# Kernel tuning notes

Measured on AMD Instinct MI355X. Metric: run time of the kernel, lower is better.

## Reference

```python
import jax, jax.numpy as jnp
import numpy as np

WINDOW_SIZE = 11
CHANNEL = 3
SIGMA = 1.5
C1 = 0.01 ** 2
C2 = 0.03 ** 2


def _gaussian_window():
    # 1D gaussian, normalized, then outer product -> [C,1,K,K] depthwise kernel
    x = np.arange(WINDOW_SIZE, dtype=np.float32)
    g = np.exp(-(x - WINDOW_SIZE // 2) ** 2 / (2.0 * SIGMA ** 2))
    g = g / g.sum()
    w2d = np.outer(g, g).astype(np.float32)  # [K,K]
    w = np.broadcast_to(w2d, (CHANNEL, 1, WINDOW_SIZE, WINDOW_SIZE)).copy()
    return jnp.asarray(w)


def _depthwise_conv(x, w):
    # x: [N,C,H,W], w: [C,1,K,K]; SAME padding (pad = K//2, K odd) matches torch
    pad = WINDOW_SIZE // 2
    return jax.lax.conv_general_dilated(
        x, w,
        window_strides=(1, 1),
        padding=((pad, pad), (pad, pad)),
        dimension_numbers=("NCHW", "OIHW", "NCHW"),
        feature_group_count=CHANNEL,
    )


def setup_inputs() -> dict:
    key = jax.random.key(0)
    kA, kB = jax.random.split(key)
    shape = (16, 3, 512, 512)
    A = jax.random.uniform(kA, shape, dtype=jnp.float32)
    B = jax.random.uniform(kB, shape, dtype=jnp.float32)
    return {"A": A, "B": B}


def reference(A, B):
    w = _gaussian_window()
    mu1 = _depthwise_conv(A, w)
    mu2 = _depthwise_conv(B, w)
    mu1_sq = mu1 * mu1
    mu2_sq = mu2 * mu2
    mu12 = mu1 * mu2
    sigma1_sq = _depthwise_conv(A * A, w) - mu1_sq
    sigma2_sq = _depthwise_conv(B * B, w) - mu2_sq
    sigma12 = _depthwise_conv(A * B, w) - mu12
    num = (2.0 * mu12 + C1) * (2.0 * sigma12 + C2)
    den = (mu1_sq + mu2_sq + C1) * (sigma1_sq + sigma2_sq + C2)
    ssim_map = num / den
    return jnp.nanmean(ssim_map)
```

## Files before the change

### kernel.cpp

```cpp
#include <hip/hip_runtime.h>
#include <math.h>


#define TX 64
#define TY 32
#define SR 42
#define HSTRIDE 65
#define IMG_H 512
#define IMG_W 512
#define C1F 1.0e-4f
#define C2F 9.0e-4f

__global__ void ssim_zero(double* acc) { *acc = 0.0; }

__global__ void ssim_finalize(const double* acc, float* out) {
    *out = (float)(*acc / 12582912.0);
}

__global__ __launch_bounds__(256, 3)
void ssim_main(const float* __restrict__ A, const float* __restrict__ B,
               double* __restrict__ acc)
{
    __shared__ float h[5][SR * HSTRIDE];

    const int t  = threadIdx.x;
    const int x0 = blockIdx.x * TX;
    const int y0 = blockIdx.y * TY;
    const size_t pbase = (size_t)blockIdx.z * (size_t)(IMG_H * IMG_W);
    const float* __restrict__ pa = A + pbase;
    const float* __restrict__ pb = B + pbase;

    float g[11];
    {
        float gs = 0.f;
        #pragma unroll
        for (int i = 0; i < 11; ++i) {
            const float d = (float)(i - 5);
            g[i] = expf(-d * d / 4.5f);
            gs += g[i];
        }
        #pragma unroll
        for (int i = 0; i < 11; ++i) g[i] /= gs;
    }

    if (t < 168) {
        const int r   = t >> 2;
        const int c0  = (t & 3) << 4;
        const int gy  = y0 - 5 + r;
        const int gxb = x0 - 5 + c0;
        const bool rowok = ((unsigned)gy < (unsigned)IMG_H);
        const float* __restrict__ ra = pa + (ptrdiff_t)gy * IMG_W;
        const float* __restrict__ rb = pb + (ptrdiff_t)gy * IMG_W;

        float a[26], b[26];
        if (rowok && gxb >= 0 && gxb + 25 < IMG_W) {
            #pragma unroll
            for (int j = 0; j < 26; ++j) {
                a[j] = ra[gxb + j];
                b[j] = rb[gxb + j];
            }
        } else {
            #pragma unroll
            for (int j = 0; j < 26; ++j) {
                const int gx = gxb + j;
                const bool ok = rowok && ((unsigned)gx < (unsigned)IMG_W);
                a[j] = ok ? ra[gx] : 0.f;
                b[j] = ok ? rb[gx] : 0.f;
            }
        }

        #pragma unroll
        for (int p = 0; p < 16; ++p) {
            float sa = 0.f, sb = 0.f, saa = 0.f, sbb = 0.f, sab = 0.f;
            #pragma unroll
            for (int k = 0; k < 11; ++k) {
                const float w  = g[k];
                const float av = a[p + k];
                const float bv = b[p + k];
                sa  += w * av;
                sb  += w * bv;
                saa += w * (av * av);
                sbb += w * (bv * bv);
                sab += w * (av * bv);
            }
            const int o = r * HSTRIDE + c0 + p;
            h[0][o] = sa;  h[1][o] = sb;
            h[2][o] = saa; h[3][o] = sbb; h[4][o] = sab;
        }
    }
    __syncthreads();

    float lsum = 0.f;
    {
        const int x  = t & 63;
        const int yb = (t >> 6) << 3;
        float m1[8], m2[8], ea[8], eb[8], ec[8];
        #pragma unroll
        for (int j = 0; j < 8; ++j) { m1[j]=0.f; m2[j]=0.f; ea[j]=0.f; eb[j]=0.f; ec[j]=0.f; }

        #pragma unroll
        for (int k = 0; k < 18; ++k) {
            const int o = (yb + k) * HSTRIDE + x;
            const float vA  = h[0][o];
            const float vB  = h[1][o];
            const float vAA = h[2][o];
            const float vBB = h[3][o];
            const float vAB = h[4][o];
            #pragma unroll
            for (int j = 0; j < 8; ++j) {
                const int kk = k - j;
                if (kk >= 0 && kk < 11) {
                    const float w = g[kk];
                    m1[j] += w * vA;  m2[j] += w * vB;
                    ea[j] += w * vAA; eb[j] += w * vBB; ec[j] += w * vAB;
                }
            }
        }

        #pragma unroll
        for (int j = 0; j < 8; ++j) {
            const float mu1 = m1[j], mu2 = m2[j];
            const float mu1s = mu1 * mu1, mu2s = mu2 * mu2, mu12 = mu1 * mu2;
            const float s1  = ea[j] - mu1s;
            const float s2  = eb[j] - mu2s;
            const float s12 = ec[j] - mu12;
            const float num = (2.f * mu12 + C1F) * (2.f * s12 + C2F);
            const float den = (mu1s + mu2s + C1F) * (s1 + s2 + C2F);
            lsum += num / den;
        }
    }

    #pragma unroll
    for (int off = 32; off > 0; off >>= 1)
        lsum += __shfl_down(lsum, off, 64);

    __syncthreads();
    if ((t & 63) == 0) h[0][t >> 6] = lsum;
    __syncthreads();
    if (t == 0) {
        const double bs = (double)h[0][0] + (double)h[0][1]
                        + (double)h[0][2] + (double)h[0][3];
        atomicAdd(acc, bs);
    }
}

extern "C" void kernel_launch(void* const* d_in, const int* in_sizes, int n_in,
                              void* d_out, int out_size, void* d_ws, size_t ws_size,
                              hipStream_t stream) {
    const float* A = (const float*)d_in[0];
    const float* B = (const float*)d_in[1];
    float* out  = (float*)d_out;
    double* acc = (double*)d_ws;

    ssim_zero<<<dim3(1), dim3(1), 0, stream>>>(acc);
    dim3 grid(IMG_W / TX, IMG_H / TY, 48);
    ssim_main<<<grid, dim3(256), 0, stream>>>(A, B, acc);
    ssim_finalize<<<dim3(1), dim3(1), 0, stream>>>(acc, out);
}
```

Before: 186.6 us.

## Retile SSIM kernel to 64x16 blocks with vectorized loads and 2x2 vertical outputs

```diff
diff --git a/kernel.cpp b/kernel.cpp
--- a/kernel.cpp
+++ b/kernel.cpp
@@ -3,11 +3,10 @@
 
 
 #define TX 64
-#define TY 32
-#define SR 42
-#define HSTRIDE 65
-#define IMG_H 512
-#define IMG_W 512
+#define TY 16
+#define SR 26
+#define LS 68
+#define IMG 512
 #define C1F 1.0e-4f
 #define C2F 9.0e-4f
 
@@ -17,16 +16,16 @@
     *out = (float)(*acc / 12582912.0);
 }
 
-__global__ __launch_bounds__(256, 3)
+__global__ __launch_bounds__(256, 4)
 void ssim_main(const float* __restrict__ A, const float* __restrict__ B,
                double* __restrict__ acc)
 {
-    __shared__ float h[5][SR * HSTRIDE];
+    __shared__ float h[5][SR * LS];
 
     const int t  = threadIdx.x;
     const int x0 = blockIdx.x * TX;
     const int y0 = blockIdx.y * TY;
-    const size_t pbase = (size_t)blockIdx.z * (size_t)(IMG_H * IMG_W);
+    const size_t pbase = (size_t)blockIdx.z * (size_t)(IMG * IMG);
     const float* __restrict__ pa = A + pbase;
     const float* __restrict__ pb = B + pbase;
 
@@ -43,90 +42,116 @@
         for (int i = 0; i < 11; ++i) g[i] /= gs;
     }
 
-    if (t < 168) {
-        const int r   = t >> 2;
-        const int c0  = (t & 3) << 4;
-        const int gy  = y0 - 5 + r;
-        const int gxb = x0 - 5 + c0;
-        const bool rowok = ((unsigned)gy < (unsigned)IMG_H);
-        const float* __restrict__ ra = pa + (ptrdiff_t)gy * IMG_W;
-        const float* __restrict__ rb = pb + (ptrdiff_t)gy * IMG_W;
+    if (t < 208) {
+        const int r  = t >> 3;
+        const int s  = t & 7;
+        const int gy = y0 - 5 + r;
+        const int xb = x0 + 8 * s;
+        const bool rowok = ((unsigned)gy < (unsigned)IMG);
+        const float* __restrict__ ra = pa + (ptrdiff_t)gy * IMG;
+        const float* __restrict__ rb = pb + (ptrdiff_t)gy * IMG;
 
-        float a[26], b[26];
-        if (rowok && gxb >= 0 && gxb + 25 < IMG_W) {
+        float wa[24], wb[24];
+        if (rowok && xb >= 8 && xb <= IMG - 16) {
+            const float4* va = (const float4*)(ra + xb - 8);
+            const float4* vb = (const float4*)(rb + xb - 8);
             #pragma unroll
-            for (int j = 0; j < 26; ++j) {
-                a[j] = ra[gxb + j];
-                b[j] = rb[gxb + j];
+            for (int q = 0; q < 6; ++q) {
+                const float4 qa = va[q], qb = vb[q];
+                wa[4*q+0] = qa.x; wa[4*q+1] = qa.y; wa[4*q+2] = qa.z; wa[4*q+3] = qa.w;
+                wb[4*q+0] = qb.x; wb[4*q+1] = qb.y; wb[4*q+2] = qb.z; wb[4*q+3] = qb.w;
             }
         } else {
             #pragma unroll
-            for (int j = 0; j < 26; ++j) {
-                const int gx = gxb + j;
-                const bool ok = rowok && ((unsigned)gx < (unsigned)IMG_W);
-                a[j] = ok ? ra[gx] : 0.f;
-                b[j] = ok ? rb[gx] : 0.f;
+            for (int i = 0; i < 24; ++i) {
+                const int gx = xb - 8 + i;
+                const bool ok = rowok && ((unsigned)gx < (unsigned)IMG);
+                wa[i] = ok ? ra[gx] : 0.f;
+                wb[i] = ok ? rb[gx] : 0.f;
             }
         }
 
+        float sa[8], sb[8], saa[8], sbb[8], sab[8];
         #pragma unroll
-        for (int p = 0; p < 16; ++p) {
-            float sa = 0.f, sb = 0.f, saa = 0.f, sbb = 0.f, sab = 0.f;
+        for (int p = 0; p < 8; ++p) { sa[p]=0.f; sb[p]=0.f; saa[p]=0.f; sbb[p]=0.f; sab[p]=0.f; }
+        #pragma unroll
+        for (int m = 0; m < 18; ++m) {
+            const float a = wa[m + 3];
+            const float b = wb[m + 3];
+            const float aa = a * a, bb = b * b, ab = a * b;
             #pragma unroll
-            for (int k = 0; k < 11; ++k) {
-                const float w  = g[k];
-                const float av = a[p + k];
-                const float bv = b[p + k];
-                sa  += w * av;
-                sb  += w * bv;
-                saa += w * (av * av);
-                sbb += w * (bv * bv);
-                sab += w * (av * bv);
+            for (int p = 0; p < 8; ++p) {
+                const int k = m - p;
+                if (k >= 0 && k <= 10) {
+                    const float w = g[k];
+                    sa[p]  += w * a;  sb[p]  += w * b;
+                    saa[p] += w * aa; sbb[p] += w * bb; sab[p] += w * ab;
+                }
             }
-            const int o = r * HSTRIDE + c0 + p;
-            h[0][o] = sa;  h[1][o] = sb;
-            h[2][o] = saa; h[3][o] = sbb; h[4][o] = sab;
         }
+        const int o = r * LS + 8 * s;
+        *(float4*)&h[0][o]   = make_float4(sa[0],  sa[1],  sa[2],  sa[3]);
+        *(float4*)&h[0][o+4] = make_float4(sa[4],  sa[5],  sa[6],  sa[7]);
+        *(float4*)&h[1][o]   = make_float4(sb[0],  sb[1],  sb[2],  sb[3]);
+        *(float4*)&h[1][o+4] = make_float4(sb[4],  sb[5],  sb[6],  sb[7]);
+        *(float4*)&h[2][o]   = make_float4(saa[0], saa[1], saa[2], saa[3]);
+        *(float4*)&h[2][o+4] = make_float4(saa[4], saa[5], saa[6], saa[7]);
+        *(float4*)&h[3][o]   = make_float4(sbb[0], sbb[1], sbb[2], sbb[3]);
+        *(float4*)&h[3][o+4] = make_float4(sbb[4], sbb[5], sbb[6], sbb[7]);
+        *(float4*)&h[4][o]   = make_float4(sab[0], sab[1], sab[2], sab[3]);
+        *(float4*)&h[4][o+4] = make_float4(sab[4], sab[5], sab[6], sab[7]);
     }
     __syncthreads();
 
     float lsum = 0.f;
     {
-        const int x  = t & 63;
-        const int yb = (t >> 6) << 3;
-        float m1[8], m2[8], ea[8], eb[8], ec[8];
+        const int xp = t & 31;
+        const int x  = xp << 1;
+        const int yb = (t >> 5) << 1;
+        float m1[2][2], m2[2][2], ea[2][2], eb[2][2], ec[2][2];
         #pragma unroll
-        for (int j = 0; j < 8; ++j) { m1[j]=0.f; m2[j]=0.f; ea[j]=0.f; eb[j]=0.f; ec[j]=0.f; }
+        for (int p = 0; p < 2; ++p)
+            #pragma unroll
+            for (int c = 0; c < 2; ++c)
+            { m1[p][c]=0.f; m2[p][c]=0.f; ea[p][c]=0.f; eb[p][c]=0.f; ec[p][c]=0.f; }
 
         #pragma unroll
-        for (int k = 0; k < 18; ++k) {
-            const int o = (yb + k) * HSTRIDE + x;
-            const float vA  = h[0][o];
-            const float vB  = h[1][o];
-            const float vAA = h[2][o];
-            const float vBB = h[3][o];
-            const float vAB = h[4][o];
+        for (int k = 0; k < 12; ++k) {
+            const int o = (yb + k) * LS + x;
+            const float2 vA  = *(const float2*)&h[0][o];
+            const float2 vB  = *(const float2*)&h[1][o];
+            const float2 vAA = *(const float2*)&h[2][o];
+            const float2 vBB = *(const float2*)&h[3][o];
+            const float2 vAB = *(const float2*)&h[4][o];
             #pragma unroll
-            for (int j = 0; j < 8; ++j) {
-                const int kk = k - j;
-                if (kk >= 0 && kk < 11) {
+            for (int p = 0; p < 2; ++p) {
+                const int kk = k - p;
+                if (kk >= 0 && kk <= 10) {
                     const float w = g[kk];
-                    m1[j] += w * vA;  m2[j] += w * vB;
-                    ea[j] += w * vAA; eb[j] += w * vBB; ec[j] += w * vAB;
+                    m1[p][0] += w * vA.x;  m1[p][1] += w * vA.y;
+                    m2[p][0] += w * vB.x;  m2[p][1] += w * vB.y;
+                    ea[p][0] += w * vAA.x; ea[p][1] += w * vAA.y;
+                    eb[p][0] += w * vBB.x; eb[p][1] += w * vBB.y;
+                    ec[p][0] += w * vAB.x; ec[p][1] += w * vAB.y;
                 }
             }
         }
 
         #pragma unroll
-        for (int j = 0; j < 8; ++j) {
-            const float mu1 = m1[j], mu2 = m2[j];
-            const float mu1s = mu1 * mu1, mu2s = mu2 * mu2, mu12 = mu1 * mu2;
-            const float s1  = ea[j] - mu1s;
-            const float s2  = eb[j] - mu2s;
-            const float s12 = ec[j] - mu12;
-            const float num = (2.f * mu12 + C1F) * (2.f * s12 + C2F);
-            const float den = (mu1s + mu2s + C1F) * (s1 + s2 + C2F);
-            lsum += num / den;
+        for (int p = 0; p < 2; ++p) {
+            #pragma unroll
+            for (int c = 0; c < 2; ++c) {
+                const float mu1 = m1[p][c], mu2 = m2[p][c];
+                const float mu1s = mu1 * mu1, mu2s = mu2 * mu2, mu12 = mu1 * mu2;
+                const float s1  = ea[p][c] - mu1s;
+                const float s2  = eb[p][c] - mu2s;
+                const float s12 = ec[p][c] - mu12;
+                const float num = (2.f * mu12 + C1F) * (2.f * s12 + C2F);
+                const float den = (mu1s + mu2s + C1F) * (s1 + s2 + C2F);
+                float rd = __builtin_amdgcn_rcpf(den);
+                rd = rd * (2.f - den * rd);
+                lsum += num * rd;
+            }
         }
     }
 
@@ -153,7 +178,7 @@
     double* acc = (double*)d_ws;
 
     ssim_zero<<<dim3(1), dim3(1), 0, stream>>>(acc);
-    dim3 grid(IMG_W / TX, IMG_H / TY, 48);
+    dim3 grid(IMG / TX, IMG / TY, 48);
     ssim_main<<<grid, dim3(256), 0, stream>>>(A, B, acc);
     ssim_finalize<<<dim3(1), dim3(1), 0, stream>>>(acc, out);
 }
```

Measured after the change: 248.3 us. 33.1% more time.
